# Kernel optimization log

Hardware: AMD Instinct MI355X
Metric: run time of the kernel (lower is better)

Reference implementation:

```python
import jax, jax.numpy as jnp
import numpy as np

N_NODES = 50000
N_EDGES = 800000
N_FEAT = 128
HIDDEN = 64
N_CLASSES = 16


def setup_inputs() -> dict:
    key = jax.random.key(0)
    ks = jax.random.split(key, 8)
    x = jax.random.normal(ks[0], (N_NODES, N_FEAT), dtype=jnp.float32)
    edge_index = jax.random.randint(ks[1], (2, N_EDGES), 0, N_NODES, dtype=jnp.int64)
    # GCNConv weights (glorot-like) and biases
    W1 = jax.random.normal(ks[2], (N_FEAT, HIDDEN), dtype=jnp.float32) / np.sqrt(N_FEAT)
    b1 = jnp.zeros((HIDDEN,), dtype=jnp.float32)
    W2 = jax.random.normal(ks[3], (HIDDEN, HIDDEN), dtype=jnp.float32) / np.sqrt(HIDDEN)
    b2 = jnp.zeros((HIDDEN,), dtype=jnp.float32)
    Wout = jax.random.normal(ks[4], (HIDDEN, N_CLASSES), dtype=jnp.float32) / np.sqrt(HIDDEN)
    bout = jnp.zeros((N_CLASSES,), dtype=jnp.float32)
    return {"x": x, "edge_index": edge_index, "W1": W1, "b1": b1,
            "W2": W2, "b2": b2, "Wout": Wout, "bout": bout}


def _gcn_conv(h, src, dst, norm, W, b, n_nodes):
    # h: [N, F_in]; linear transform then normalized scatter-add aggregation
    h = h @ W                                   # [N, F_out]
    msg = h[src] * norm[:, None]                # gather + scale  [E+N, F_out]
    out = jax.ops.segment_sum(msg, dst, num_segments=n_nodes)  # scatter-add
    return out + b


def reference(x, edge_index, W1, b1, W2, b2, Wout, bout):
    n = x.shape[0]
    # add self-loops (PyG GCNConv default add_self_loops=True)
    loops = jnp.arange(n, dtype=edge_index.dtype)
    src = jnp.concatenate([edge_index[0], loops])
    dst = jnp.concatenate([edge_index[1], loops])
    # symmetric normalization: deg^-1/2[src] * deg^-1/2[dst] (edge_weight = 1)
    ones = jnp.ones(src.shape[0], dtype=x.dtype)
    deg = jax.ops.segment_sum(ones, dst, num_segments=n)
    dinv = jnp.where(deg > 0, jax.lax.rsqrt(jnp.maximum(deg, 1e-12)), 0.0)
    norm = dinv[src] * dinv[dst]

    h = _gcn_conv(x, src, dst, norm, W1, b1, n)
    h = jax.nn.relu(h)
    # dropout p=0.5 with training=False -> identity
    h = _gcn_conv(h, src, dst, norm, W2, b2, n)
    h = jax.nn.relu(h)
    logits = h @ Wout + bout
    return jax.nn.softmax(logits, axis=1)
```

## Files before the change

### kernel.cpp

```cpp
#include <hip/hip_runtime.h>
#include <hip/hip_fp16.h>

#define N_NODES 50000
#define N_EDGES 800000
#define N_FEAT 128
#define HIDDEN 64
#define N_CLASSES 16
#define NBLK_NODE 196
#define TCAP 8192

typedef _Float16 f16x8 __attribute__((ext_vector_type(8)));
typedef float f32x4 __attribute__((ext_vector_type(4)));

__global__ void k_init(int* __restrict__ tileCur) {
    int tid = threadIdx.x;
    if (tid < NBLK_NODE) tileCur[tid] = tid * TCAP;
}

__global__ __launch_bounds__(256) void k_part(const int* __restrict__ ei,
                                              int* __restrict__ tileCur,
                                              int* __restrict__ binned) {
    __shared__ int cnt[NBLK_NODE], base[NBLK_NODE], cur[NBLK_NODE];
    int tid = threadIdx.x;
    int start = blockIdx.x * 4096;
    if (tid < NBLK_NODE) cnt[tid] = 0;
    __syncthreads();
    int s[16], d[16];
#pragma unroll
    for (int u = 0; u < 4; ++u) {
        int e0 = start + u * 1024 + tid * 4;
        if (e0 + 4 <= N_EDGES) {
            int4 s4 = *(const int4*)&ei[e0];
            int4 d4 = *(const int4*)&ei[N_EDGES + e0];
            s[u * 4 + 0] = s4.x; s[u * 4 + 1] = s4.y; s[u * 4 + 2] = s4.z; s[u * 4 + 3] = s4.w;
            d[u * 4 + 0] = d4.x; d[u * 4 + 1] = d4.y; d[u * 4 + 2] = d4.z; d[u * 4 + 3] = d4.w;
#pragma unroll
            for (int q = 0; q < 4; ++q) atomicAdd(&cnt[d[u * 4 + q] >> 8], 1);
        } else {
#pragma unroll
            for (int q = 0; q < 4; ++q) {
                int e = e0 + q;
                if (e < N_EDGES) {
                    s[u * 4 + q] = ei[e];
                    d[u * 4 + q] = ei[N_EDGES + e];
                    atomicAdd(&cnt[d[u * 4 + q] >> 8], 1);
                } else s[u * 4 + q] = -1;
            }
        }
    }
    __syncthreads();
    if (tid < NBLK_NODE) {
        base[tid] = atomicAdd(&tileCur[tid], cnt[tid]);
        cur[tid] = 0;
    }
    __syncthreads();
#pragma unroll
    for (int u = 0; u < 16; ++u) {
        if (s[u] < 0) continue;
        int t = d[u] >> 8;
        int r = atomicAdd(&cur[t], 1);
        int p = base[t] + r;
        if (p < (t + 1) * TCAP)
            binned[p] = s[u] | ((d[u] & 255) << 16);
    }
}

__device__ __forceinline__ void finesort_body(int tb, const int* __restrict__ binned,
                                              const int* __restrict__ tileCur,
                                              int* __restrict__ csr,
                                              int2* __restrict__ rse,
                                              float* __restrict__ dinv, char* smem) {
    int* stage   = (int*)smem;
    int* sc      = stage + TCAP;
    int* cnt256  = sc + 256;
    int* nodeOff = cnt256 + 256;
    int tid = threadIdx.x;
    int beg = tb * TCAP;
    int m = tileCur[tb] - beg;
    if (m > TCAP) m = TCAP;
    cnt256[tid] = 0;
    __syncthreads();
    const int4* b4 = (const int4*)(binned + beg);
    int nv = m >> 2;
    for (int i = tid; i < nv; i += 256) {
        int4 r = b4[i];
        atomicAdd(&cnt256[(r.x >> 16) & 255], 1);
        atomicAdd(&cnt256[(r.y >> 16) & 255], 1);
        atomicAdd(&cnt256[(r.z >> 16) & 255], 1);
        atomicAdd(&cnt256[(r.w >> 16) & 255], 1);
    }
    for (int i = (m & ~3) + tid; i < m; i += 256)
        atomicAdd(&cnt256[(binned[beg + i] >> 16) & 255], 1);
    __syncthreads();
    int myc = cnt256[tid];
    sc[tid] = myc;
    __syncthreads();
#pragma unroll
    for (int off = 1; off < 256; off <<= 1) {
        int t = (tid >= off) ? sc[tid - off] : 0;
        __syncthreads();
        sc[tid] += t;
        __syncthreads();
    }
    int off0 = sc[tid] - myc;
    nodeOff[tid] = off0;
    int gnode = tb * 256 + tid;
    if (gnode < N_NODES) {
        dinv[gnode] = rsqrtf((float)myc + 1.0f);
        rse[gnode] = make_int2(beg + off0, myc);
    }
    cnt256[tid] = 0;
    __syncthreads();
    for (int i = tid; i < nv; i += 256) {
        int4 r = b4[i];
        int rr;
        rr = atomicAdd(&cnt256[(r.x >> 16) & 255], 1); stage[nodeOff[(r.x >> 16) & 255] + rr] = r.x & 0xFFFF;
        rr = atomicAdd(&cnt256[(r.y >> 16) & 255], 1); stage[nodeOff[(r.y >> 16) & 255] + rr] = r.y & 0xFFFF;
        rr = atomicAdd(&cnt256[(r.z >> 16) & 255], 1); stage[nodeOff[(r.z >> 16) & 255] + rr] = r.z & 0xFFFF;
        rr = atomicAdd(&cnt256[(r.w >> 16) & 255], 1); stage[nodeOff[(r.w >> 16) & 255] + rr] = r.w & 0xFFFF;
    }
    for (int i = (m & ~3) + tid; i < m; i += 256) {
        int rec = binned[beg + i];
        int dl = (rec >> 16) & 255;
        int rr = atomicAdd(&cnt256[dl], 1);
        stage[nodeOff[dl] + rr] = rec & 0xFFFF;
    }
    __syncthreads();
    int4* c4 = (int4*)(csr + beg);
    for (int i = tid; i < nv; i += 256) c4[i] = ((const int4*)stage)[i];
    for (int i = (m & ~3) + tid; i < m; i += 256) csr[beg + i] = stage[i];
}

template <int K, typename TIn>
__device__ __forceinline__ void mm_body(int bx, const TIn* __restrict__ a,
                                        const float* __restrict__ w,
                                        const float* __restrict__ dscale,
                                        __half* __restrict__ out, char* smem) {
    constexpr int LDK = K + 8;
    __half* A_lds  = (__half*)smem;
    __half* Wt_lds = A_lds + 64 * LDK;
    int tid = threadIdx.x;
    long nbase = (long)bx * 64;

    for (int i = tid; i < K * 16; i += 256) {
        int k = (i * 4) >> 6;
        int f0 = (i * 4) & 63;
        float4 v = *(const float4*)&w[i * 4];
        Wt_lds[(f0 + 0) * LDK + k] = __float2half(v.x);
        Wt_lds[(f0 + 1) * LDK + k] = __float2half(v.y);
        Wt_lds[(f0 + 2) * LDK + k] = __float2half(v.z);
        Wt_lds[(f0 + 3) * LDK + k] = __float2half(v.w);
    }
    for (int i = tid; i < 64 * K / 8; i += 256) {
        int n = (i * 8) / K;
        int k0 = (i * 8) % K;
        long gn = nbase + n;
        if constexpr (sizeof(TIn) == 4) {
            float4 v0, v1;
            if (gn < N_NODES) {
                v0 = *(const float4*)&a[gn * K + k0];
                v1 = *(const float4*)&a[gn * K + k0 + 4];
            } else {
                v0 = make_float4(0.f, 0.f, 0.f, 0.f);
                v1 = v0;
            }
            __half2* dst = (__half2*)&A_lds[n * LDK + k0];
            dst[0] = __floats2half2_rn(v0.x, v0.y);
            dst[1] = __floats2half2_rn(v0.z, v0.w);
            dst[2] = __floats2half2_rn(v1.x, v1.y);
            dst[3] = __floats2half2_rn(v1.z, v1.w);
        } else {
            int4 v = (gn < N_NODES) ? *(const int4*)&a[gn * K + k0]
                                    : make_int4(0, 0, 0, 0);
            *(int4*)&A_lds[n * LDK + k0] = v;
        }
    }
    __syncthreads();

    int wv = tid >> 6;
    int lane = tid & 63;
    int m = lane & 15;
    int quad = lane >> 4;
    const __half* Arow = &A_lds[(wv * 16 + m) * LDK + quad * 8];
    f32x4 acc[4] = {};
#pragma unroll
    for (int t = 0; t < K; t += 32) {
        f16x8 af = *(const f16x8*)(const void*)&Arow[t];
#pragma unroll
        for (int g = 0; g < 4; ++g) {
            f16x8 bf = *(const f16x8*)(const void*)&Wt_lds[(g * 16 + m) * LDK + t + quad * 8];
            acc[g] = __builtin_amdgcn_mfma_f32_16x16x32_f16(af, bf, acc[g], 0, 0, 0);
        }
    }

#pragma unroll
    for (int r = 0; r < 4; ++r) {
        int n = wv * 16 + quad * 4 + r;
        long gn = nbase + n;
        if (gn < N_NODES) {
            float di = dscale ? dscale[gn] : 1.0f;
#pragma unroll
            for (int g = 0; g < 4; ++g)
                out[gn * HIDDEN + g * 16 + m] = __float2half(acc[g][r] * di);
        }
    }
}

__global__ __launch_bounds__(256) void k_fsmm1(const int* __restrict__ binned,
                                               const int* __restrict__ tileCur,
                                               int* __restrict__ csr,
                                               int2* __restrict__ rse,
                                               float* __restrict__ dinv,
                                               const float* __restrict__ x,
                                               const float* __restrict__ W1,
                                               __half* __restrict__ bufA) {
    __shared__ __align__(16) char smem[35840];
    int bx = blockIdx.x;
    if (bx < NBLK_NODE)
        finesort_body(bx, binned, tileCur, csr, rse, dinv, smem);
    else
        mm_body<N_FEAT, float>(bx - NBLK_NODE, x, W1, nullptr, bufA, smem);
}

__global__ __launch_bounds__(256) void k_mm2(const __half* __restrict__ a,
                                             const float* __restrict__ w,
                                             const float* __restrict__ dinv,
                                             __half* __restrict__ out) {
    __shared__ __align__(16) char smem[2 * 64 * (HIDDEN + 8) * 2];
    mm_body<HIDDEN, __half>(blockIdx.x, a, w, dinv, out, smem);
}

__device__ __forceinline__ void acc_row8s(float* a, int4 rv, float s) {
    float2 f;
    f = __half22float2(*(__half2*)&rv.x); a[0] = fmaf(f.x, s, a[0]); a[1] = fmaf(f.y, s, a[1]);
    f = __half22float2(*(__half2*)&rv.y); a[2] = fmaf(f.x, s, a[2]); a[3] = fmaf(f.y, s, a[3]);
    f = __half22float2(*(__half2*)&rv.z); a[4] = fmaf(f.x, s, a[4]); a[5] = fmaf(f.y, s, a[5]);
    f = __half22float2(*(__half2*)&rv.w); a[6] = fmaf(f.x, s, a[6]); a[7] = fmaf(f.y, s, a[7]);
}
__device__ __forceinline__ void acc_row8(float* a, int4 rv) {
    float2 f;
    f = __half22float2(*(__half2*)&rv.x); a[0] += f.x; a[1] += f.y;
    f = __half22float2(*(__half2*)&rv.y); a[2] += f.x; a[3] += f.y;
    f = __half22float2(*(__half2*)&rv.z); a[4] += f.x; a[5] += f.y;
    f = __half22float2(*(__half2*)&rv.w); a[6] += f.x; a[7] += f.y;
}

template <bool SCALE>
__global__ void k_gather(const __half* __restrict__ h, const int* __restrict__ csr,
                         const int2* __restrict__ rse, const float* __restrict__ dinv,
                         const float* __restrict__ bias, __half* __restrict__ out) {
    int t = blockIdx.x * 256 + threadIdx.x;
    int node = __builtin_amdgcn_readfirstlane(t >> 6);
    int lane = t & 63;
    int e8 = lane >> 3;
    int q = lane & 7;

    int4 vs = make_int4(0, 0, 0, 0);
    if (e8 == 0) vs = *(const int4*)&h[(long)node * HIDDEN + q * 8];
    float dd = dinv[node];
    int2 se = rse[node];
    int r0 = se.x, deg = se.y;

    bool p0 = e8 < deg, p1 = e8 + 8 < deg, p2 = e8 + 16 < deg, p3 = e8 + 24 < deg;
    int c0 = 0, c1 = 0, c2 = 0, c3 = 0;
    if (p0) c0 = csr[r0 + e8];
    if (p1) c1 = csr[r0 + 8 + e8];
    if (p2) c2 = csr[r0 + 16 + e8];
    if (p3) c3 = csr[r0 + 24 + e8];

    int4 v0 = make_int4(0,0,0,0), v1 = v0, v2 = v0, v3 = v0;
    float d0 = 0.f, d1 = 0.f, d2 = 0.f, d3 = 0.f;
    if (p0) { v0 = *(const int4*)&h[(long)c0 * HIDDEN + q * 8]; if (SCALE) d0 = dinv[c0]; }
    if (p1) { v1 = *(const int4*)&h[(long)c1 * HIDDEN + q * 8]; if (SCALE) d1 = dinv[c1]; }
    if (p2) { v2 = *(const int4*)&h[(long)c2 * HIDDEN + q * 8]; if (SCALE) d2 = dinv[c2]; }
    if (p3) { v3 = *(const int4*)&h[(long)c3 * HIDDEN + q * 8]; if (SCALE) d3 = dinv[c3]; }

    float a[8] = {0.f, 0.f, 0.f, 0.f, 0.f, 0.f, 0.f, 0.f};
    if constexpr (SCALE) {
        acc_row8s(a, vs, dd);
        acc_row8s(a, v0, d0);
        acc_row8s(a, v1, d1);
        acc_row8s(a, v2, d2);
        acc_row8s(a, v3, d3);
    } else {
        acc_row8(a, vs);
        acc_row8(a, v0);
        acc_row8(a, v1);
        acc_row8(a, v2);
        acc_row8(a, v3);
    }

    for (int j = 32; j < deg; j += 8) {
        if (j + e8 < deg) {
            int s = csr[r0 + j + e8];
            int4 rv = *(const int4*)&h[(long)s * HIDDEN + q * 8];
            if constexpr (SCALE) acc_row8s(a, rv, dinv[s]);
            else                 acc_row8(a, rv);
        }
    }

#pragma unroll
    for (int off = 8; off < 64; off <<= 1)
#pragma unroll
        for (int i = 0; i < 8; ++i) a[i] += __shfl_xor(a[i], off, 64);

    if (e8 == 0) {
        float4 b0 = *(const float4*)&bias[q * 8];
        float4 b1 = *(const float4*)&bias[q * 8 + 4];
        float r[8];
        r[0] = fmaxf(fmaf(a[0], dd, b0.x), 0.f);
        r[1] = fmaxf(fmaf(a[1], dd, b0.y), 0.f);
        r[2] = fmaxf(fmaf(a[2], dd, b0.z), 0.f);
        r[3] = fmaxf(fmaf(a[3], dd, b0.w), 0.f);
        r[4] = fmaxf(fmaf(a[4], dd, b1.x), 0.f);
        r[5] = fmaxf(fmaf(a[5], dd, b1.y), 0.f);
        r[6] = fmaxf(fmaf(a[6], dd, b1.z), 0.f);
        r[7] = fmaxf(fmaf(a[7], dd, b1.w), 0.f);
        __half2 h0 = __floats2half2_rn(r[0], r[1]);
        __half2 h1 = __floats2half2_rn(r[2], r[3]);
        __half2 h2 = __floats2half2_rn(r[4], r[5]);
        __half2 h3 = __floats2half2_rn(r[6], r[7]);
        int4 o;
        o.x = *(int*)&h0; o.y = *(int*)&h1; o.z = *(int*)&h2; o.w = *(int*)&h3;
        *(int4*)&out[(long)node * HIDDEN + q * 8] = o;
    }
}

__global__ void k_out(const __half* __restrict__ h, const float* __restrict__ w,
                      const float* __restrict__ b, float* __restrict__ out) {
    __shared__ float Ws[HIDDEN * N_CLASSES];
    __shared__ float bs[N_CLASSES];
    int tid = threadIdx.x;
    for (int i = tid; i < HIDDEN * N_CLASSES; i += 256) Ws[i] = w[i];
    if (tid < N_CLASSES) bs[tid] = b[tid];
    __syncthreads();
    int node = blockIdx.x * 16 + (tid >> 4);
    int c = tid & 15;
    const __half* hr = h + (long)node * HIDDEN;
    float acc = bs[c];
#pragma unroll
    for (int k = 0; k < HIDDEN; ++k)
        acc = fmaf(__half2float(hr[k]), Ws[k * N_CLASSES + c], acc);
    float m = acc;
#pragma unroll
    for (int off = 8; off; off >>= 1) m = fmaxf(m, __shfl_xor(m, off, 16));
    float ex = expf(acc - m);
    float s = ex;
#pragma unroll
    for (int off = 8; off; off >>= 1) s += __shfl_xor(s, off, 16);
    out[(long)node * N_CLASSES + c] = ex / s;
}

extern "C" void kernel_launch(void* const* d_in, const int* in_sizes, int n_in,
                              void* d_out, int out_size, void* d_ws, size_t ws_size,
                              hipStream_t stream) {
    const float* x    = (const float*)d_in[0];
    const int*   ei   = (const int*)d_in[1];
    const float* W1   = (const float*)d_in[2];
    const float* b1   = (const float*)d_in[3];
    const float* W2   = (const float*)d_in[4];
    const float* b2   = (const float*)d_in[5];
    const float* Wout = (const float*)d_in[6];
    const float* bout = (const float*)d_in[7];
    float* out = (float*)d_out;

    char* ws = (char*)d_ws;
    int2*   rse     = (int2*)ws;                       ws += 400128;
    float*  dinv    = (float*)ws;                      ws += 200192;
    int*    tileCur = (int*)ws;                        ws += 1024;
    int*    csr     = (int*)ws;                        ws += (size_t)NBLK_NODE * TCAP * 4;
    int*    binned  = (int*)ws;                        ws += (size_t)NBLK_NODE * TCAP * 4;
    __half* bufA    = (__half*)ws;                     ws += 6553600;
    __half* bufB    = (__half*)ws;

    const int NB_MM = (N_NODES + 63) / 64;
    const int NB_E16 = (N_EDGES + 4095) / 4096;

    k_init<<<1, 256, 0, stream>>>(tileCur);
    k_part<<<NB_E16, 256, 0, stream>>>(ei, tileCur, binned);

    k_fsmm1<<<NBLK_NODE + NB_MM, 256, 0, stream>>>(binned, tileCur, csr, rse, dinv,
                                                   x, W1, bufA);

    k_gather<true><<<N_NODES / 4, 256, 0, stream>>>(bufA, csr, rse, dinv, b1, bufB);

    k_mm2<<<NB_MM, 256, 0, stream>>>(bufB, W2, dinv, bufA);
    k_gather<false><<<N_NODES / 4, 256, 0, stream>>>(bufA, csr, rse, dinv, b2, bufB);

    k_out<<<N_NODES / 16, 256, 0, stream>>>(bufB, Wout, bout, out);
}
```

Measured before the change: 164.7 us.

## Single-pass counting sort in finesort with wave-shuffle prefix scan

The per-tile fine sort now keeps the loaded records and their atomic ranks in registers from the counting pass and reuses them for placement. This removes the second read of the binned data and the second round of LDS atomics. The 256-entry block scan moves from a log-step LDS scan with many barriers to a 64-lane shuffle scan plus a small cross-wave sum, which cuts both barriers and LDS use. In exchange it uses more registers (64 ints per thread), which could lower occupancy of the fused kernel.

```diff
diff --git a/kernel.cpp b/kernel.cpp
--- a/kernel.cpp
+++ b/kernel.cpp
@@ -71,9 +71,9 @@
                                               int2* __restrict__ rse,
                                               float* __restrict__ dinv, char* smem) {
     int* stage   = (int*)smem;
-    int* sc      = stage + TCAP;
-    int* cnt256  = sc + 256;
+    int* cnt256  = stage + TCAP;
     int* nodeOff = cnt256 + 256;
+    int* wsum    = nodeOff + 256;
     int tid = threadIdx.x;
     int beg = tb * TCAP;
     int m = tileCur[tb] - beg;
@@ -82,49 +82,60 @@
     __syncthreads();
     const int4* b4 = (const int4*)(binned + beg);
     int nv = m >> 2;
-    for (int i = tid; i < nv; i += 256) {
-        int4 r = b4[i];
-        atomicAdd(&cnt256[(r.x >> 16) & 255], 1);
-        atomicAdd(&cnt256[(r.y >> 16) & 255], 1);
-        atomicAdd(&cnt256[(r.z >> 16) & 255], 1);
-        atomicAdd(&cnt256[(r.w >> 16) & 255], 1);
-    }
-    for (int i = (m & ~3) + tid; i < m; i += 256)
-        atomicAdd(&cnt256[(binned[beg + i] >> 16) & 255], 1);
+    int4 v[8], rk[8];
+#pragma unroll
+    for (int u = 0; u < 8; ++u) {
+        int i = tid + u * 256;
+        if (i < nv) {
+            int4 r = b4[i];
+            v[u] = r;
+            rk[u].x = atomicAdd(&cnt256[(r.x >> 16) & 255], 1);
+            rk[u].y = atomicAdd(&cnt256[(r.y >> 16) & 255], 1);
+            rk[u].z = atomicAdd(&cnt256[(r.z >> 16) & 255], 1);
+            rk[u].w = atomicAdd(&cnt256[(r.w >> 16) & 255], 1);
+        }
+    }
+    int trec = -1, trk = 0;
+    int ti = (m & ~3) + tid;
+    if (ti < m) {
+        trec = binned[beg + ti];
+        trk = atomicAdd(&cnt256[(trec >> 16) & 255], 1);
+    }
     __syncthreads();
     int myc = cnt256[tid];
-    sc[tid] = myc;
-    __syncthreads();
-#pragma unroll
-    for (int off = 1; off < 256; off <<= 1) {
-        int t = (tid >= off) ? sc[tid - off] : 0;
-        __syncthreads();
-        sc[tid] += t;
-        __syncthreads();
-    }
-    int off0 = sc[tid] - myc;
+    int sc = myc;
+#pragma unroll
+    for (int off = 1; off < 64; off <<= 1) {
+        int t2 = __shfl_up(sc, off, 64);
+        if ((tid & 63) >= off) sc += t2;
+    }
+    if ((tid & 63) == 63) wsum[tid >> 6] = sc;
+    __syncthreads();
+    int wv = tid >> 6;
+    int pre = 0;
+    if (wv > 0) pre += wsum[0];
+    if (wv > 1) pre += wsum[1];
+    if (wv > 2) pre += wsum[2];
+    int off0 = sc - myc + pre;
     nodeOff[tid] = off0;
     int gnode = tb * 256 + tid;
     if (gnode < N_NODES) {
         dinv[gnode] = rsqrtf((float)myc + 1.0f);
         rse[gnode] = make_int2(beg + off0, myc);
     }
-    cnt256[tid] = 0;
-    __syncthreads();
-    for (int i = tid; i < nv; i += 256) {
-        int4 r = b4[i];
-        int rr;
-        rr = atomicAdd(&cnt256[(r.x >> 16) & 255], 1); stage[nodeOff[(r.x >> 16) & 255] + rr] = r.x & 0xFFFF;
-        rr = atomicAdd(&cnt256[(r.y >> 16) & 255], 1); stage[nodeOff[(r.y >> 16) & 255] + rr] = r.y & 0xFFFF;
-        rr = atomicAdd(&cnt256[(r.z >> 16) & 255], 1); stage[nodeOff[(r.z >> 16) & 255] + rr] = r.z & 0xFFFF;
-        rr = atomicAdd(&cnt256[(r.w >> 16) & 255], 1); stage[nodeOff[(r.w >> 16) & 255] + rr] = r.w & 0xFFFF;
-    }
-    for (int i = (m & ~3) + tid; i < m; i += 256) {
-        int rec = binned[beg + i];
-        int dl = (rec >> 16) & 255;
-        int rr = atomicAdd(&cnt256[dl], 1);
-        stage[nodeOff[dl] + rr] = rec & 0xFFFF;
-    }
+    __syncthreads();
+#pragma unroll
+    for (int u = 0; u < 8; ++u) {
+        int i = tid + u * 256;
+        if (i < nv) {
+            stage[nodeOff[(v[u].x >> 16) & 255] + rk[u].x] = v[u].x & 0xFFFF;
+            stage[nodeOff[(v[u].y >> 16) & 255] + rk[u].y] = v[u].y & 0xFFFF;
+            stage[nodeOff[(v[u].z >> 16) & 255] + rk[u].z] = v[u].z & 0xFFFF;
+            stage[nodeOff[(v[u].w >> 16) & 255] + rk[u].w] = v[u].w & 0xFFFF;
+        }
+    }
+    if (trec >= 0)
+        stage[nodeOff[(trec >> 16) & 255] + trk] = trec & 0xFFFF;
     __syncthreads();
     int4* c4 = (int4*)(csr + beg);
     for (int i = tid; i < nv; i += 256) c4[i] = ((const int4*)stage)[i];
@@ -214,7 +225,7 @@
                                                const float* __restrict__ x,
                                                const float* __restrict__ W1,
                                                __half* __restrict__ bufA) {
-    __shared__ __align__(16) char smem[35840];
+    __shared__ __align__(16) char smem[34832];
     int bx = blockIdx.x;
     if (bx < NBLK_NODE)
         finesort_body(bx, binned, tileCur, csr, rse, dinv, smem);
```

Result: no change. 163.4 us (-0.8%).
